# Performance work log

Measured on AMD Instinct MI355X. Metric: run time of the kernel, lower is better.

The kernel has to match this reference:

```python
import jax, jax.numpy as jnp
import numpy as np

N = 50000      # nodes
E = 800000     # edges (avg degree 16)
IN = 128       # in_channels
H = 8          # heads (layer 1)
C = 32         # hidden_channels per head
OUT = 40       # out_channels + 1
NEG_SLOPE = 0.2  # PyG GATConv default


def glorot(key, shape, fan_in, fan_out):
    lim = np.sqrt(6.0 / (fan_in + fan_out)).astype(np.float32)
    return jax.random.uniform(key, shape, jnp.float32, -lim, lim)


def setup_inputs() -> dict:
    key = jax.random.key(0)
    ks = jax.random.split(key, 10)
    x = jax.random.normal(ks[0], (N, IN), jnp.float32)
    edge_index = jax.random.randint(ks[1], (2, E), 0, N, dtype=jnp.int32)
    # layer 1: in -> H*C, heads=8, concat
    W1 = glorot(ks[2], (IN, H * C), IN, H * C)
    att_src1 = glorot(ks[3], (H, C), C, C)
    att_dst1 = glorot(ks[4], (H, C), C, C)
    b1 = jnp.zeros((H * C,), jnp.float32)
    # layer 2: H*C -> OUT, heads=1
    W2 = glorot(ks[5], (H * C, OUT), H * C, OUT)
    att_src2 = glorot(ks[6], (1, OUT), OUT, OUT)
    att_dst2 = glorot(ks[7], (1, OUT), OUT, OUT)
    b2 = jnp.zeros((OUT,), jnp.float32)
    return {"x": x, "edge_index": edge_index, "W1": W1, "att_src1": att_src1,
            "att_dst1": att_dst1, "b1": b1, "W2": W2, "att_src2": att_src2,
            "att_dst2": att_dst2, "b2": b2}


def gat_conv(x, edge_index, W, att_src, att_dst, bias):
    # PyG GATConv (eval mode, add_self_loops=True, concat=True)
    n = x.shape[0]
    heads, ch = att_src.shape
    loop = jnp.arange(n, dtype=edge_index.dtype)
    src = jnp.concatenate([edge_index[0], loop])  # message source j
    dst = jnp.concatenate([edge_index[1], loop])  # message target i
    h = (x @ W).reshape(n, heads, ch)                       # [N,H,C]
    a_src = jnp.einsum('nhc,hc->nh', h, att_src)            # [N,H]
    a_dst = jnp.einsum('nhc,hc->nh', h, att_dst)            # [N,H]
    logits = jax.nn.leaky_relu(a_src[src] + a_dst[dst], NEG_SLOPE)  # [Et,H]
    # segmented softmax over incoming edges of each target node
    m = jax.ops.segment_max(logits, dst, num_segments=n)    # [N,H]
    p = jnp.exp(logits - m[dst])
    s = jax.ops.segment_sum(p, dst, num_segments=n)         # [N,H]
    alpha = p / s[dst]                                      # [Et,H]
    msg = h[src] * alpha[:, :, None]                        # [Et,H,C]
    out = jax.ops.segment_sum(msg, dst, num_segments=n)     # [N,H,C]
    return out.reshape(n, heads * ch) + bias


def reference(x, edge_index, W1, att_src1, att_dst1, b1, W2, att_src2, att_dst2, b2):
    h = gat_conv(x, edge_index, W1, att_src1, att_dst1, b1)
    h = jax.nn.relu(h)  # dropout is identity in eval mode
    h = gat_conv(h, edge_index, W2, att_src2, att_dst2, b2)
    return jax.nn.log_softmax(h, axis=1)
```

## Files before the change

kernel.cpp:

```cpp
#include <hip/hip_runtime.h>
#include <hip/hip_bf16.h>
#include <math.h>

#define NEG_SLOPE 0.2f

__device__ __forceinline__ float lrelu(float x){ return x > 0.f ? x : NEG_SLOPE * x; }
__device__ __forceinline__ unsigned short f2bf(float f){
  __hip_bfloat16 h = __float2bfloat16(f);
  return __builtin_bit_cast(unsigned short, h);
}
__device__ __forceinline__ float b2f(unsigned short u){
  return __builtin_bit_cast(float, (unsigned)u << 16);
}

typedef short bf16x8 __attribute__((ext_vector_type(8)));
typedef float f32x4 __attribute__((ext_vector_type(4)));

__global__ void k_count(const int* __restrict__ dst, int* __restrict__ deg, int E){
  int e = blockIdx.x*256 + threadIdx.x;
  if (e < E) atomicAdd(&deg[dst[e]], 1);
}

__global__ __launch_bounds__(256) void k_scan1(const int* __restrict__ deg, int* __restrict__ bsum, int n){
  int tid = threadIdx.x;
  int base = blockIdx.x*1024 + tid*4;
  int s = 0;
  #pragma unroll
  for (int j=0;j<4;j++){ int idx = base+j; if (idx < n) s += deg[idx]; }
  #pragma unroll
  for (int off=32; off; off>>=1) s += __shfl_xor(s, off);
  __shared__ int ws[4];
  if ((tid&63)==0) ws[tid>>6] = s;
  __syncthreads();
  if (tid==0) bsum[blockIdx.x] = ws[0]+ws[1]+ws[2]+ws[3];
}

__global__ void k_scan2(const int* __restrict__ bsum, int* __restrict__ boff,
                        int* __restrict__ rowptr, int nb, int n){
  int lane = threadIdx.x;
  int v = (lane < nb) ? bsum[lane] : 0;
  int inc = v;
  #pragma unroll
  for (int off=1; off<64; off<<=1){ int t = __shfl_up(inc, off); if (lane >= off) inc += t; }
  if (lane < nb) boff[lane] = inc - v;
  if (lane == 63) rowptr[n] = inc;
}

__global__ __launch_bounds__(256) void k_scan3(const int* __restrict__ deg, const int* __restrict__ boff,
    int* __restrict__ rowptr, int* __restrict__ nxt, int n){
  int tid = threadIdx.x; int lane = tid & 63, w = tid >> 6;
  int base = blockIdx.x*1024 + tid*4;
  int v[4]; int s = 0;
  #pragma unroll
  for (int j=0;j<4;j++){ int idx = base+j; v[j] = (idx < n) ? deg[idx] : 0; s += v[j]; }
  int inc = s;
  #pragma unroll
  for (int off=1; off<64; off<<=1){ int t = __shfl_up(inc, off); if (lane >= off) inc += t; }
  __shared__ int ws[4];
  if (lane == 63) ws[w] = inc;
  __syncthreads();
  int run = boff[blockIdx.x];
  for (int ww=0; ww<w; ww++) run += ws[ww];
  run += inc - s;
  #pragma unroll
  for (int j=0;j<4;j++){ int idx = base+j; if (idx < n){ rowptr[idx] = run; nxt[idx] = run; run += v[j]; } }
}

__global__ void k_scatter(const int* __restrict__ src, const int* __restrict__ dst,
                          int* __restrict__ nxt, int* __restrict__ srcs, int E){
  int e = blockIdx.x*256 + threadIdx.x;
  if (e < E){
    int pos = atomicAdd(&nxt[dst[e]], 1);
    srcs[pos] = src[e];
  }
}

__global__ void k_wt(const float* __restrict__ W, unsigned short* __restrict__ Wt, int NCreal){
  int c = blockIdx.x, k = threadIdx.x, K = blockDim.x;
  float v = (c < NCreal) ? W[(size_t)k*NCreal + c] : 0.f;
  Wt[(size_t)c*K + k] = f2bf(v);
}

__global__ __launch_bounds__(256) void gemm1_att(
    const float* __restrict__ x, const unsigned short* __restrict__ Bt,
    unsigned short* __restrict__ C, const float* __restrict__ att_s,
    const float* __restrict__ att_d, float* __restrict__ asrc,
    float* __restrict__ adst, int M){
  __shared__ unsigned short sA[64][40];
  __shared__ unsigned short sB[256][40];
  const int tid = threadIdx.x;
  const int wid = tid >> 6, lane = tid & 63;
  const int r0 = blockIdx.x * 64;
  const int fr = lane & 15, fk = (lane >> 4) * 8;
  f32x4 acc[4][4] = {};

  for (int k0 = 0; k0 < 128; k0 += 32){
    #pragma unroll
    for (int t=0; t<2; t++){
      int id = tid + t*256;
      int r = id >> 3, q = id & 7;
      float4 v = make_float4(0.f,0.f,0.f,0.f);
      int row = r0 + r;
      if (row < M) v = ((const float4*)(x + (size_t)row*128))[(k0>>2) + q];
      ushort4 o; o.x=f2bf(v.x); o.y=f2bf(v.y); o.z=f2bf(v.z); o.w=f2bf(v.w);
      *(ushort4*)&sA[r][q*4] = o;
    }
    #pragma unroll
    for (int t=0; t<4; t++){
      int id = tid + t*256;
      int r = id >> 2, lk = (id & 3) * 8;
      uint4 vb = *(const uint4*)(Bt + (size_t)r*128 + k0 + lk);
      *(uint4*)&sB[r][lk] = vb;
    }
    __syncthreads();
    bf16x8 a[4], b[4];
    #pragma unroll
    for (int mi=0; mi<4; mi++) a[mi] = *(const bf16x8*)&sA[mi*16 + fr][fk];
    #pragma unroll
    for (int ni=0; ni<4; ni++) b[ni] = *(const bf16x8*)&sB[wid*64 + ni*16 + fr][fk];
    #pragma unroll
    for (int mi=0; mi<4; mi++)
      #pragma unroll
      for (int ni=0; ni<4; ni++)
        acc[mi][ni] = __builtin_amdgcn_mfma_f32_16x16x32_bf16(a[mi], b[ni], acc[mi][ni], 0,0,0);
    __syncthreads();
  }

  float avs[4], avd[4];
  #pragma unroll
  for (int ni=0; ni<4; ni++){
    int idx = (2*wid + (ni>>1))*32 + (ni&1)*16 + fr;
    avs[ni] = att_s[idx];
    avd[ni] = att_d[idx];
  }

  #pragma unroll
  for (int mi=0; mi<4; mi++){
    #pragma unroll
    for (int j=0; j<4; j++){
      int row = r0 + mi*16 + (lane>>4)*4 + j;
      #pragma unroll
      for (int ni=0; ni<4; ni++){
        int col = wid*64 + ni*16 + fr;
        if (row < M) C[(size_t)row*256 + col] = f2bf(acc[mi][ni][j]);
      }
      float s0 = acc[mi][0][j]*avs[0] + acc[mi][1][j]*avs[1];
      float s1 = acc[mi][2][j]*avs[2] + acc[mi][3][j]*avs[3];
      float d0 = acc[mi][0][j]*avd[0] + acc[mi][1][j]*avd[1];
      float d1 = acc[mi][2][j]*avd[2] + acc[mi][3][j]*avd[3];
      #pragma unroll
      for (int mk=1; mk<16; mk<<=1){
        s0 += __shfl_xor(s0, mk); s1 += __shfl_xor(s1, mk);
        d0 += __shfl_xor(d0, mk); d1 += __shfl_xor(d1, mk);
      }
      if ((lane & 15) == 0 && row < M){
        asrc[(size_t)row*8 + 2*wid    ] = s0;
        asrc[(size_t)row*8 + 2*wid + 1] = s1;
        adst[(size_t)row*8 + 2*wid    ] = d0;
        adst[(size_t)row*8 + 2*wid + 1] = d1;
      }
    }
  }
}

__global__ __launch_bounds__(256) void gemm_mfma(
    const unsigned short* __restrict__ A, const unsigned short* __restrict__ Bt,
    unsigned short* __restrict__ C, int M, int K, int ldc){
  __shared__ unsigned short sA[64][40];
  __shared__ unsigned short sB[64][40];
  const int tid = threadIdx.x;
  const int wid = tid >> 6, lane = tid & 63;
  const int r0 = blockIdx.x * 64, c0 = blockIdx.y * 64;
  const int wr = wid >> 1, wc = wid & 1;
  const int lr = tid >> 2;
  const int lk = (tid & 3) * 8;
  const int fr = lane & 15, fk = (lane >> 4) * 8;
  f32x4 acc[2][2] = {};

  for (int k0 = 0; k0 < K; k0 += 32){
    uint4 va = make_uint4(0,0,0,0);
    int row = r0 + lr;
    if (row < M) va = *(const uint4*)(A + (size_t)row*K + k0 + lk);
    *(uint4*)&sA[lr][lk] = va;
    uint4 vb = *(const uint4*)(Bt + (size_t)(c0 + lr)*K + k0 + lk);
    *(uint4*)&sB[lr][lk] = vb;
    __syncthreads();
    bf16x8 a0 = *(const bf16x8*)&sA[wr*32 + fr][fk];
    bf16x8 a1 = *(const bf16x8*)&sA[wr*32 + 16 + fr][fk];
    bf16x8 b0 = *(const bf16x8*)&sB[wc*32 + fr][fk];
    bf16x8 b1 = *(const bf16x8*)&sB[wc*32 + 16 + fr][fk];
    acc[0][0] = __builtin_amdgcn_mfma_f32_16x16x32_bf16(a0, b0, acc[0][0], 0,0,0);
    acc[0][1] = __builtin_amdgcn_mfma_f32_16x16x32_bf16(a0, b1, acc[0][1], 0,0,0);
    acc[1][0] = __builtin_amdgcn_mfma_f32_16x16x32_bf16(a1, b0, acc[1][0], 0,0,0);
    acc[1][1] = __builtin_amdgcn_mfma_f32_16x16x32_bf16(a1, b1, acc[1][1], 0,0,0);
    __syncthreads();
  }
  #pragma unroll
  for (int mi=0; mi<2; mi++){
    int rowb = r0 + wr*32 + mi*16 + (lane>>4)*4;
    #pragma unroll
    for (int ni=0; ni<2; ni++){
      int col = c0 + wc*32 + ni*16 + fr;
      #pragma unroll
      for (int j=0;j<4;j++){
        int row = rowb + j;
        if (row < M) C[(size_t)row*ldc + col] = f2bf(acc[mi][ni][j]);
      }
    }
  }
}

__global__ void k_att2(const unsigned short* __restrict__ h, const float* __restrict__ att_s,
    const float* __restrict__ att_d, float* __restrict__ asrc, float* __restrict__ adst, int n){
  int id = blockIdx.x*256 + threadIdx.x;
  if (id >= n) return;
  const unsigned short* hv = h + (size_t)id*64;
  float s = 0.f, d = 0.f;
  #pragma unroll
  for (int q=0; q<5; q++){
    ushort4 u0 = ((const ushort4*)hv)[q*2];
    ushort4 u1 = ((const ushort4*)hv)[q*2+1];
    float v0=b2f(u0.x), v1=b2f(u0.y), v2=b2f(u0.z), v3=b2f(u0.w);
    float v4=b2f(u1.x), v5=b2f(u1.y), v6=b2f(u1.z), v7=b2f(u1.w);
    float4 a0 = ((const float4*)att_s)[q*2], a1 = ((const float4*)att_s)[q*2+1];
    float4 d0 = ((const float4*)att_d)[q*2], d1 = ((const float4*)att_d)[q*2+1];
    s += v0*a0.x + v1*a0.y + v2*a0.z + v3*a0.w + v4*a1.x + v5*a1.y + v6*a1.z + v7*a1.w;
    d += v0*d0.x + v1*d0.y + v2*d0.z + v3*d0.w + v4*d1.x + v5*d1.y + v6*d1.z + v7*d1.w;
  }
  asrc[id] = s; adst[id] = d;
}

__global__ __launch_bounds__(256) void k_agg1(
    const unsigned short* __restrict__ h1, const float* __restrict__ asrc,
    const float* __restrict__ adst, const int* __restrict__ rowptr,
    const int* __restrict__ srcs, const float* __restrict__ bias,
    unsigned short* __restrict__ zb, int n){
  int i = (blockIdx.x*256 + threadIdx.x) >> 6;
  int lane = threadIdx.x & 63;
  if (i >= n) return;
  int hd = lane >> 3;
  float adsti = adst[(size_t)i*8 + hd];
  float pself = __expf(lrelu(asrc[(size_t)i*8 + hd] + adsti));
  float ssum = pself;
  uint2 hs = ((const uint2*)(h1 + (size_t)i*256))[lane];
  float4 acc;
  acc.x = pself * b2f((unsigned short)(hs.x & 0xffff));
  acc.y = pself * b2f((unsigned short)(hs.x >> 16));
  acc.z = pself * b2f((unsigned short)(hs.y & 0xffff));
  acc.w = pself * b2f((unsigned short)(hs.y >> 16));
  int e0 = rowptr[i], e1 = rowptr[i+1];
  int e = e0;
  for (; e + 8 <= e1; e += 8){
    int sx[8]; uint2 vv[8]; float pp[8];
    #pragma unroll
    for (int j=0;j<8;j++) sx[j] = srcs[e+j];
    #pragma unroll
    for (int j=0;j<8;j++) vv[j] = ((const uint2*)(h1 + (size_t)sx[j]*256))[lane];
    #pragma unroll
    for (int j=0;j<8;j++) pp[j] = __expf(lrelu(asrc[(size_t)sx[j]*8 + hd] + adsti));
    #pragma unroll
    for (int j=0;j<8;j++){
      float p = pp[j];
      ssum += p;
      acc.x += p * b2f((unsigned short)(vv[j].x & 0xffff));
      acc.y += p * b2f((unsigned short)(vv[j].x >> 16));
      acc.z += p * b2f((unsigned short)(vv[j].y & 0xffff));
      acc.w += p * b2f((unsigned short)(vv[j].y >> 16));
    }
  }
  for (; e < e1; ++e){
    int s = srcs[e];
    uint2 v = ((const uint2*)(h1 + (size_t)s*256))[lane];
    float p = __expf(lrelu(asrc[(size_t)s*8 + hd] + adsti));
    ssum += p;
    acc.x += p * b2f((unsigned short)(v.x & 0xffff));
    acc.y += p * b2f((unsigned short)(v.x >> 16));
    acc.z += p * b2f((unsigned short)(v.y & 0xffff));
    acc.w += p * b2f((unsigned short)(v.y >> 16));
  }
  float inv = 1.f / ssum;
  float4 b = ((const float4*)bias)[lane];
  ushort4 ob;
  ob.x = f2bf(fmaxf(fmaf(acc.x, inv, b.x), 0.f));
  ob.y = f2bf(fmaxf(fmaf(acc.y, inv, b.y), 0.f));
  ob.z = f2bf(fmaxf(fmaf(acc.z, inv, b.z), 0.f));
  ob.w = f2bf(fmaxf(fmaf(acc.w, inv, b.w), 0.f));
  ((ushort4*)(zb + (size_t)i*256))[lane] = ob;
}

__global__ __launch_bounds__(256) void k_agg2(
    const unsigned short* __restrict__ h2, const float* __restrict__ asrc,
    const float* __restrict__ adst, const int* __restrict__ rowptr,
    const int* __restrict__ srcs, const float* __restrict__ bias,
    float* __restrict__ out, int n){
  int wid = (blockIdx.x*256 + threadIdx.x) >> 6;
  int lane = threadIdx.x & 63;
  if (wid >= n) return;
  int i = wid;
  bool act = lane < 40;
  float adsti = adst[i];
  float pself = __expf(lrelu(asrc[i] + adsti));
  float ssum = pself;
  float acc = pself * b2f(h2[(size_t)i*64 + lane]);
  int e0 = rowptr[i], e1 = rowptr[i+1];
  int e = e0;
  for (; e + 8 <= e1; e += 8){
    int sx[8]; float vv[8], pp[8];
    #pragma unroll
    for (int j=0;j<8;j++) sx[j] = srcs[e+j];
    #pragma unroll
    for (int j=0;j<8;j++) vv[j] = b2f(h2[(size_t)sx[j]*64 + lane]);
    #pragma unroll
    for (int j=0;j<8;j++) pp[j] = __expf(lrelu(asrc[sx[j]] + adsti));
    #pragma unroll
    for (int j=0;j<8;j++){
      ssum += pp[j];
      acc += pp[j] * vv[j];
    }
  }
  for (; e < e1; ++e){
    int s = srcs[e];
    float v = b2f(h2[(size_t)s*64 + lane]);
    float p = __expf(lrelu(asrc[s] + adsti));
    ssum += p;
    acc += p * v;
  }
  float val = act ? (acc/ssum + bias[lane]) : -INFINITY;
  float mx = val;
  #pragma unroll
  for (int off=32; off; off>>=1) mx = fmaxf(mx, __shfl_xor(mx, off));
  float ex = act ? __expf(val - mx) : 0.f;
  float se = ex;
  #pragma unroll
  for (int off=32; off; off>>=1) se += __shfl_xor(se, off);
  if (act) out[(size_t)i*40 + lane] = val - mx - __logf(se);
}

extern "C" void kernel_launch(void* const* d_in, const int* in_sizes, int n_in,
                              void* d_out, int out_size, void* d_ws, size_t ws_size,
                              hipStream_t stream){
  const float* x   = (const float*)d_in[0];
  const int*   ei  = (const int*)d_in[1];
  const float* W1  = (const float*)d_in[2];
  const float* as1 = (const float*)d_in[3];
  const float* ad1 = (const float*)d_in[4];
  const float* b1  = (const float*)d_in[5];
  const float* W2  = (const float*)d_in[6];
  const float* as2 = (const float*)d_in[7];
  const float* ad2 = (const float*)d_in[8];
  const float* b2  = (const float*)d_in[9];
  float* out = (float*)d_out;

  const int N = in_sizes[0] / 128;
  const int E = in_sizes[1] / 2;
  const int* srcI = ei;
  const int* dstI = ei + E;

  char* ws = (char*)d_ws;
  size_t off = 0;
  auto alloc = [&](size_t bytes){ void* p = ws + off; off += (bytes + 255) & ~(size_t)255; return p; };
  unsigned short* h1b = (unsigned short*)alloc((size_t)N*256*2);
  unsigned short* zb  = (unsigned short*)alloc((size_t)N*256*2);
  unsigned short* h2b = (unsigned short*)alloc((size_t)N*64*2);
  unsigned short* W1t = (unsigned short*)alloc((size_t)256*128*2);
  unsigned short* W2t = (unsigned short*)alloc((size_t)64*256*2);
  float* asrc1 = (float*)alloc((size_t)N*8*4);
  float* adst1 = (float*)alloc((size_t)N*8*4);
  float* asrc2 = (float*)alloc((size_t)N*4);
  float* adst2 = (float*)alloc((size_t)N*4);
  int* deg     = (int*)alloc((size_t)N*4);
  int* rowptr  = (int*)alloc((size_t)(N+1)*4);
  int* nxt     = (int*)alloc((size_t)N*4);
  int* srcs    = (int*)alloc((size_t)E*4);
  int* bsum    = (int*)alloc(256*4);
  int* boff    = (int*)alloc(256*4);
  (void)ws_size; (void)n_in; (void)out_size;

  const int nb = (N + 1023)/1024;
  hipMemsetAsync(deg, 0, (size_t)N*4, stream);
  int eb = (E + 255)/256;
  k_count <<<eb, 256, 0, stream>>>(dstI, deg, E);
  k_scan1 <<<nb, 256, 0, stream>>>(deg, bsum, N);
  k_scan2 <<<1, 64, 0, stream>>>(bsum, boff, rowptr, nb, N);
  k_scan3 <<<nb, 256, 0, stream>>>(deg, boff, rowptr, nxt, N);
  k_scatter<<<eb, 256, 0, stream>>>(srcI, dstI, nxt, srcs, E);

  k_wt <<<256, 128, 0, stream>>>(W1, W1t, 256);
  k_wt <<<64, 256, 0, stream>>>(W2, W2t, 40);

  gemm1_att<<<(N + 63)/64, 256, 0, stream>>>(x, W1t, h1b, as1, ad1, asrc1, adst1, N);
  k_agg1<<<(N + 3)/4, 256, 0, stream>>>(h1b, asrc1, adst1, rowptr, srcs, b1, zb, N);

  dim3 g2((N + 63)/64, 1);
  gemm_mfma<<<g2, 256, 0, stream>>>(zb, W2t, h2b, N, 256, 64);
  k_att2<<<(N + 255)/256, 256, 0, stream>>>(h2b, as2, ad2, asrc2, adst2, N);
  k_agg2<<<(N + 3)/4, 256, 0, stream>>>(h2b, asrc2, adst2, rowptr, srcs, b2, out, N);
}
```

Before: 324.7 us.

## Precompute per-edge attention weights in separate edge kernels before aggregation

Adds dst storage to the CSR scatter and two new per-edge kernels that compute exp(leaky_relu(asrc+adst)) for each edge. Layer 1 stores these as bf16 and layer 2 as fp32, in CSR order. The aggregation kernels then read these contiguous weights instead of gathering asrc for every lane, and the scalar tail loops become a single masked 8-wide batch. In exchange the change adds two kernel launches, extra writes and reads of edge-sized buffers, and bf16 rounding of the layer-1 attention weights.

```diff
diff --git a/kernel.cpp b/kernel.cpp
--- a/kernel.cpp
+++ b/kernel.cpp
@@ -67,11 +67,14 @@
 }
 
 __global__ void k_scatter(const int* __restrict__ src, const int* __restrict__ dst,
-                          int* __restrict__ nxt, int* __restrict__ srcs, int E){
+                          int* __restrict__ nxt, int* __restrict__ srcs,
+                          int* __restrict__ dsts, int E){
   int e = blockIdx.x*256 + threadIdx.x;
   if (e < E){
-    int pos = atomicAdd(&nxt[dst[e]], 1);
+    int d = dst[e];
+    int pos = atomicAdd(&nxt[d], 1);
     srcs[pos] = src[e];
+    dsts[pos] = d;
   }
 }
 
@@ -79,6 +82,26 @@
   int c = blockIdx.x, k = threadIdx.x, K = blockDim.x;
   float v = (c < NCreal) ? W[(size_t)k*NCreal + c] : 0.f;
   Wt[(size_t)c*K + k] = f2bf(v);
+}
+
+__global__ void k_edgep1(const int* __restrict__ srcs, const int* __restrict__ dsts,
+    const float* __restrict__ asrc, const float* __restrict__ adst,
+    unsigned short* __restrict__ p1, int E8){
+  int id = blockIdx.x*256 + threadIdx.x;
+  if (id >= E8) return;
+  int pos = id >> 3, hd = id & 7;
+  int s = srcs[pos], d = dsts[pos];
+  float l = lrelu(asrc[(size_t)s*8 + hd] + adst[(size_t)d*8 + hd]);
+  p1[id] = f2bf(__expf(l));
+}
+
+__global__ void k_edgep2(const int* __restrict__ srcs, const int* __restrict__ dsts,
+    const float* __restrict__ asrc, const float* __restrict__ adst,
+    float* __restrict__ p2, int E){
+  int pos = blockIdx.x*256 + threadIdx.x;
+  if (pos >= E) return;
+  int s = srcs[pos], d = dsts[pos];
+  p2[pos] = __expf(lrelu(asrc[s] + adst[d]));
 }
 
 __global__ __launch_bounds__(256) void gemm1_att(
@@ -233,14 +256,13 @@
 __global__ __launch_bounds__(256) void k_agg1(
     const unsigned short* __restrict__ h1, const float* __restrict__ asrc,
     const float* __restrict__ adst, const int* __restrict__ rowptr,
-    const int* __restrict__ srcs, const float* __restrict__ bias,
-    unsigned short* __restrict__ zb, int n){
+    const int* __restrict__ srcs, const unsigned short* __restrict__ p1,
+    const float* __restrict__ bias, unsigned short* __restrict__ zb, int n){
   int i = (blockIdx.x*256 + threadIdx.x) >> 6;
   int lane = threadIdx.x & 63;
   if (i >= n) return;
   int hd = lane >> 3;
-  float adsti = adst[(size_t)i*8 + hd];
-  float pself = __expf(lrelu(asrc[(size_t)i*8 + hd] + adsti));
+  float pself = __expf(lrelu(asrc[(size_t)i*8 + hd] + adst[(size_t)i*8 + hd]));
   float ssum = pself;
   uint2 hs = ((const uint2*)(h1 + (size_t)i*256))[lane];
   float4 acc;
@@ -249,18 +271,18 @@
   acc.z = pself * b2f((unsigned short)(hs.y & 0xffff));
   acc.w = pself * b2f((unsigned short)(hs.y >> 16));
   int e0 = rowptr[i], e1 = rowptr[i+1];
-  int e = e0;
-  for (; e + 8 <= e1; e += 8){
-    int sx[8]; uint2 vv[8]; float pp[8];
+  int efull = e0 + ((e1 - e0) & ~7);
+  for (int e = e0; e < efull; e += 8){
+    int sx[8]; uint2 vv[8]; float pv[8];
     #pragma unroll
     for (int j=0;j<8;j++) sx[j] = srcs[e+j];
     #pragma unroll
     for (int j=0;j<8;j++) vv[j] = ((const uint2*)(h1 + (size_t)sx[j]*256))[lane];
     #pragma unroll
-    for (int j=0;j<8;j++) pp[j] = __expf(lrelu(asrc[(size_t)sx[j]*8 + hd] + adsti));
-    #pragma unroll
-    for (int j=0;j<8;j++){
-      float p = pp[j];
+    for (int j=0;j<8;j++) pv[j] = b2f(p1[(size_t)(e+j)*8 + hd]);
+    #pragma unroll
+    for (int j=0;j<8;j++){
+      float p = pv[j];
       ssum += p;
       acc.x += p * b2f((unsigned short)(vv[j].x & 0xffff));
       acc.y += p * b2f((unsigned short)(vv[j].x >> 16));
@@ -268,15 +290,27 @@
       acc.w += p * b2f((unsigned short)(vv[j].y >> 16));
     }
   }
-  for (; e < e1; ++e){
-    int s = srcs[e];
-    uint2 v = ((const uint2*)(h1 + (size_t)s*256))[lane];
-    float p = __expf(lrelu(asrc[(size_t)s*8 + hd] + adsti));
-    ssum += p;
-    acc.x += p * b2f((unsigned short)(v.x & 0xffff));
-    acc.y += p * b2f((unsigned short)(v.x >> 16));
-    acc.z += p * b2f((unsigned short)(v.y & 0xffff));
-    acc.w += p * b2f((unsigned short)(v.y >> 16));
+  if (efull < e1){
+    int sx[8]; uint2 vv[8]; float pv[8];
+    #pragma unroll
+    for (int j=0;j<8;j++){
+      int ee = efull + j;
+      int idx = ee < e1 ? ee : e1 - 1;
+      sx[j] = srcs[idx];
+      unsigned short pr = p1[(size_t)idx*8 + hd];
+      pv[j] = (ee < e1) ? b2f(pr) : 0.f;
+    }
+    #pragma unroll
+    for (int j=0;j<8;j++) vv[j] = ((const uint2*)(h1 + (size_t)sx[j]*256))[lane];
+    #pragma unroll
+    for (int j=0;j<8;j++){
+      float p = pv[j];
+      ssum += p;
+      acc.x += p * b2f((unsigned short)(vv[j].x & 0xffff));
+      acc.y += p * b2f((unsigned short)(vv[j].x >> 16));
+      acc.z += p * b2f((unsigned short)(vv[j].y & 0xffff));
+      acc.w += p * b2f((unsigned short)(vv[j].y >> 16));
+    }
   }
   float inv = 1.f / ssum;
   float4 b = ((const float4*)bias)[lane];
@@ -291,39 +325,49 @@
 __global__ __launch_bounds__(256) void k_agg2(
     const unsigned short* __restrict__ h2, const float* __restrict__ asrc,
     const float* __restrict__ adst, const int* __restrict__ rowptr,
-    const int* __restrict__ srcs, const float* __restrict__ bias,
-    float* __restrict__ out, int n){
+    const int* __restrict__ srcs, const float* __restrict__ p2,
+    const float* __restrict__ bias, float* __restrict__ out, int n){
   int wid = (blockIdx.x*256 + threadIdx.x) >> 6;
   int lane = threadIdx.x & 63;
   if (wid >= n) return;
   int i = wid;
   bool act = lane < 40;
-  float adsti = adst[i];
-  float pself = __expf(lrelu(asrc[i] + adsti));
+  float pself = __expf(lrelu(asrc[i] + adst[i]));
   float ssum = pself;
   float acc = pself * b2f(h2[(size_t)i*64 + lane]);
   int e0 = rowptr[i], e1 = rowptr[i+1];
-  int e = e0;
-  for (; e + 8 <= e1; e += 8){
-    int sx[8]; float vv[8], pp[8];
+  int efull = e0 + ((e1 - e0) & ~7);
+  for (int e = e0; e < efull; e += 8){
+    int sx[8]; float vv[8], pv[8];
     #pragma unroll
     for (int j=0;j<8;j++) sx[j] = srcs[e+j];
     #pragma unroll
     for (int j=0;j<8;j++) vv[j] = b2f(h2[(size_t)sx[j]*64 + lane]);
     #pragma unroll
-    for (int j=0;j<8;j++) pp[j] = __expf(lrelu(asrc[sx[j]] + adsti));
-    #pragma unroll
-    for (int j=0;j<8;j++){
-      ssum += pp[j];
-      acc += pp[j] * vv[j];
-    }
-  }
-  for (; e < e1; ++e){
-    int s = srcs[e];
-    float v = b2f(h2[(size_t)s*64 + lane]);
-    float p = __expf(lrelu(asrc[s] + adsti));
-    ssum += p;
-    acc += p * v;
+    for (int j=0;j<8;j++) pv[j] = p2[e+j];
+    #pragma unroll
+    for (int j=0;j<8;j++){
+      ssum += pv[j];
+      acc += pv[j] * vv[j];
+    }
+  }
+  if (efull < e1){
+    int sx[8]; float vv[8], pv[8];
+    #pragma unroll
+    for (int j=0;j<8;j++){
+      int ee = efull + j;
+      int idx = ee < e1 ? ee : e1 - 1;
+      sx[j] = srcs[idx];
+      float pr = p2[idx];
+      pv[j] = (ee < e1) ? pr : 0.f;
+    }
+    #pragma unroll
+    for (int j=0;j<8;j++) vv[j] = b2f(h2[(size_t)sx[j]*64 + lane]);
+    #pragma unroll
+    for (int j=0;j<8;j++){
+      ssum += pv[j];
+      acc += pv[j] * vv[j];
+    }
   }
   float val = act ? (acc/ssum + bias[lane]) : -INFINITY;
   float mx = val;
@@ -364,6 +408,8 @@
   unsigned short* h2b = (unsigned short*)alloc((size_t)N*64*2);
   unsigned short* W1t = (unsigned short*)alloc((size_t)256*128*2);
   unsigned short* W2t = (unsigned short*)alloc((size_t)64*256*2);
+  unsigned short* p1  = (unsigned short*)alloc((size_t)E*8*2);
+  float* p2    = (float*)alloc((size_t)E*4);
   float* asrc1 = (float*)alloc((size_t)N*8*4);
   float* adst1 = (float*)alloc((size_t)N*8*4);
   float* asrc2 = (float*)alloc((size_t)N*4);
@@ -372,6 +418,7 @@
   int* rowptr  = (int*)alloc((size_t)(N+1)*4);
   int* nxt     = (int*)alloc((size_t)N*4);
   int* srcs    = (int*)alloc((size_t)E*4);
+  int* dsts    = (int*)alloc((size_t)E*4);
   int* bsum    = (int*)alloc(256*4);
   int* boff    = (int*)alloc(256*4);
   (void)ws_size; (void)n_in; (void)out_size;
@@ -383,16 +430,18 @@
   k_scan1 <<<nb, 256, 0, stream>>>(deg, bsum, N);
   k_scan2 <<<1, 64, 0, stream>>>(bsum, boff, rowptr, nb, N);
   k_scan3 <<<nb, 256, 0, stream>>>(deg, boff, rowptr, nxt, N);
-  k_scatter<<<eb, 256, 0, stream>>>(srcI, dstI, nxt, srcs, E);
+  k_scatter<<<eb, 256, 0, stream>>>(srcI, dstI, nxt, srcs, dsts, E);
 
   k_wt <<<256, 128, 0, stream>>>(W1, W1t, 256);
   k_wt <<<64, 256, 0, stream>>>(W2, W2t, 40);
 
   gemm1_att<<<(N + 63)/64, 256, 0, stream>>>(x, W1t, h1b, as1, ad1, asrc1, adst1, N);
-  k_agg1<<<(N + 3)/4, 256, 0, stream>>>(h1b, asrc1, adst1, rowptr, srcs, b1, zb, N);
+  k_edgep1<<<(E*8 + 255)/256, 256, 0, stream>>>(srcs, dsts, asrc1, adst1, p1, E*8);
+  k_agg1<<<(N + 3)/4, 256, 0, stream>>>(h1b, asrc1, adst1, rowptr, srcs, p1, b1, zb, N);
 
   dim3 g2((N + 63)/64, 1);
   gemm_mfma<<<g2, 256, 0, stream>>>(zb, W2t, h2b, N, 256, 64);
   k_att2<<<(N + 255)/256, 256, 0, stream>>>(h2b, as2, ad2, asrc2, adst2, N);
-  k_agg2<<<(N + 3)/4, 256, 0, stream>>>(h2b, asrc2, adst2, rowptr, srcs, b2, out, N);
-}
+  k_edgep2<<<eb, 256, 0, stream>>>(srcs, dsts, asrc2, adst2, p2, E);
+  k_agg2<<<(N + 3)/4, 256, 0, stream>>>(h2b, asrc2, adst2, rowptr, srcs, p2, b2, out, N);
+}
```

After: 329.9 us. Within noise of the previous version (+1.6%).
